# Performance work log

Hardware: AMD Instinct MI355X
Metric: run time of the kernel (lower is better)

Reference implementation:

```python
import jax, jax.numpy as jnp
import numpy as np

D_MODEL = 768
N_HEAD = 12

def setup_inputs() -> dict:
    key = jax.random.key(0)
    ks = jax.random.split(key, 5)
    B, T, C = 2, 2048, D_MODEL
    s = 1.0 / np.sqrt(C)
    x = jax.random.normal(ks[0], (B, T, C), dtype=jnp.float32)
    W_attn = jax.random.normal(ks[1], (C, 3 * C), dtype=jnp.float32) * s
    b_attn = jnp.zeros((3 * C,), dtype=jnp.float32)
    W_proj = jax.random.normal(ks[2], (C, C), dtype=jnp.float32) * s
    b_proj = jnp.zeros((C,), dtype=jnp.float32)
    return {"x": x, "W_attn": W_attn, "b_attn": b_attn, "W_proj": W_proj, "b_proj": b_proj}

def reference(x, W_attn, b_attn, W_proj, b_proj):
    B, T, C = x.shape
    H, Dh = N_HEAD, C // N_HEAD
    qkv = x @ W_attn + b_attn  # [B,T,3C]
    q, k, v = jnp.split(qkv, 3, axis=-1)
    q = q.reshape(B, T, H, Dh).transpose(0, 2, 1, 3)  # [B,H,T,Dh]
    k = k.reshape(B, T, H, Dh).transpose(0, 2, 1, 3)
    v = v.reshape(B, T, H, Dh).transpose(0, 2, 1, 3)
    att = jnp.einsum('bhqd,bhkd->bhqk', q, k) * (1.0 / np.sqrt(Dh))
    mask = jnp.tril(jnp.ones((T, T), dtype=bool))  # causal
    att = jnp.where(mask, att, -jnp.inf)
    att = jax.nn.softmax(att, axis=-1)
    y = jnp.einsum('bhqk,bhkd->bhqd', att, v)
    y = y.transpose(0, 2, 1, 3).reshape(B, T, C)
    return y @ W_proj + b_proj
```

## Files before the change

### kernel.cpp

```cpp
#include <hip/hip_runtime.h>
#include <hip/hip_bf16.h>
#include <math.h>

#define BB 2
#define TT 2048
#define CC 768
#define HH 12
#define DD 64
#define KD 768
#define NCH 80

#define QSCALE 0.18033688011112044f
#define THR2 11.5f

typedef __attribute__((ext_vector_type(8))) short bf16x8;
typedef __attribute__((ext_vector_type(4))) float f32x4;
typedef __attribute__((ext_vector_type(4))) float f32x4v;
typedef __attribute__((ext_vector_type(4))) ushort u16x4;

static __device__ __forceinline__ ushort f2bf(float f) {
  union { float f; unsigned u; } v; v.f = f;
  unsigned r = v.u + 0x7FFF + ((v.u >> 16) & 1);
  return (ushort)(r >> 16);
}
static __device__ __forceinline__ float bf2f(ushort u) {
  union { unsigned u; float f; } v; v.u = ((unsigned)u) << 16;
  return v.f;
}

#define NB_CVT 3072
#define NB_TA  1728
#define NB_TP  576

__global__ __launch_bounds__(256) void prep_fused(
    const float* __restrict__ x, ushort* __restrict__ xb,
    const float* __restrict__ Wa, ushort* __restrict__ Wat,
    const float* __restrict__ Wp, ushort* __restrict__ Wpt) {
  const int bid = blockIdx.x;
  const int tid = threadIdx.x;
  if (bid < NB_CVT) {
    const int i = bid * 256 + tid;
    f32x4v v = ((const f32x4v*)x)[i];
    u16x4 o;
    o.x = f2bf(v.x); o.y = f2bf(v.y); o.z = f2bf(v.z); o.w = f2bf(v.w);
    ((u16x4*)xb)[i] = o;
    return;
  }
  __shared__ float t[32][33];
  const float* W; ushort* Wt; int N, idx;
  if (bid < NB_CVT + NB_TA) { W = Wa; Wt = Wat; N = 3 * CC; idx = bid - NB_CVT; }
  else                      { W = Wp; Wt = Wpt; N = CC;     idx = bid - NB_CVT - NB_TA; }
  const int ntx = N / 32;
  const int n0 = (idx % ntx) * 32, k0 = (idx / ntx) * 32;
  const int tx = tid & 31, ty = tid >> 5;
#pragma unroll
  for (int j = 0; j < 32; j += 8)
    t[ty + j][tx] = W[(size_t)(k0 + ty + j) * N + n0 + tx];
  __syncthreads();
#pragma unroll
  for (int j = 0; j < 32; j += 8)
    Wt[(size_t)(n0 + ty + j) * KD + k0 + tx] = f2bf(t[tx][ty + j]);
}

__global__ __launch_bounds__(256) void gemm_mfma(
    const ushort* __restrict__ A, const ushort* __restrict__ Bt,
    const float* __restrict__ bias, int N, int mode,
    ushort* __restrict__ Qo, ushort* __restrict__ Ko, ushort* __restrict__ Vo,
    float* __restrict__ Of) {
  __shared__ ushort As[128 * 32];
  __shared__ ushort Bs[128 * 32];
  const int tid = threadIdx.x;
  const int w = tid >> 6, lane = tid & 63;
  const int wr = w >> 1, wc = w & 1;
  const int grp = lane >> 4, colk = lane & 15;
  const int bm = blockIdx.y * 128, bn = blockIdx.x * 128;

  f32x4 acc[4][4] = {};

  auto* AsL = (__attribute__((address_space(3))) char*)As;
  auto* BsL = (__attribute__((address_space(3))) char*)Bs;

  for (int k0 = 0; k0 < KD; k0 += 32) {
#pragma unroll
    for (int i = 0; i < 2; ++i) {
      const int idx = tid + i * 256;
      const int row = idx >> 2, g = idx & 3;
      const int eoff = (g * 8) ^ ((row & 3) << 3);
      const ushort* sa = A + (size_t)(bm + row) * KD + k0 + eoff;
      const ushort* sb = Bt + (size_t)(bn + row) * KD + k0 + eoff;
      __builtin_amdgcn_global_load_lds(
          (const __attribute__((address_space(1))) void*)sa,
          (__attribute__((address_space(3))) void*)(AsL + w * 1024 + i * 4096), 16, 0, 0);
      __builtin_amdgcn_global_load_lds(
          (const __attribute__((address_space(1))) void*)sb,
          (__attribute__((address_space(3))) void*)(BsL + w * 1024 + i * 4096), 16, 0, 0);
    }
    __syncthreads();

    bf16x8 af[4], bf[4];
    const int sw = (colk & 3) << 3;
#pragma unroll
    for (int m = 0; m < 4; ++m)
      af[m] = *(const bf16x8*)&As[(wr * 64 + m * 16 + colk) * 32 + ((grp * 8) ^ sw)];
#pragma unroll
    for (int n = 0; n < 4; ++n)
      bf[n] = *(const bf16x8*)&Bs[(wc * 64 + n * 16 + colk) * 32 + ((grp * 8) ^ sw)];
#pragma unroll
    for (int m = 0; m < 4; ++m)
#pragma unroll
      for (int n = 0; n < 4; ++n)
        acc[m][n] = __builtin_amdgcn_mfma_f32_16x16x32_bf16(af[m], bf[n], acc[m][n], 0, 0, 0);
    __syncthreads();
  }

#pragma unroll
  for (int m = 0; m < 4; ++m) {
    const int gro = bm + wr * 64 + m * 16 + grp * 4;
#pragma unroll
    for (int n = 0; n < 4; ++n) {
      const int col = bn + wc * 64 + n * 16 + colk;
      const float bv = bias[col];
#pragma unroll
      for (int j = 0; j < 4; ++j) {
        const int row = gro + j;
        float v = acc[m][n][j] + bv;
        if (mode == 0) {
          const int which = col / CC;
          const int c = col - which * CC;
          const int hh = c >> 6, d = c & 63;
          const int b = row >> 11, t = row & 2047;
          if (which == 0) v *= QSCALE;
          const ushort bvv = f2bf(v);
          if (which == 0)
            Qo[((size_t)((b * HH + hh) * TT + t)) * DD + d] = bvv;
          else if (which == 1)
            Ko[((size_t)((b * HH + hh) * TT + t)) * DD + d] = bvv;
          else
            Vo[((size_t)((b * HH + hh) * DD + d)) * TT + t] = bvv;
        } else {
          Of[(size_t)row * N + col] = v;
        }
      }
    }
  }
}

__global__ __launch_bounds__(256) void attn_mfma(
    const ushort* __restrict__ Q, const ushort* __restrict__ K,
    const ushort* __restrict__ Vt, ushort* __restrict__ Po,
    float* __restrict__ Pml) {
  const int c = NCH - 1 - (int)blockIdx.x;
  int qq, ci;
  if (c < 8)       { qq = c;                              ci = 0; }
  else if (c < 24) { int o_ = c - 8;  qq = 8  + (o_ >> 1); ci = o_ & 1; }
  else if (c < 48) { int o_ = c - 24; qq = 16 + o_ / 3;    ci = o_ % 3; }
  else             { int o_ = c - 48; qq = 24 + (o_ >> 2); ci = o_ & 3; }
  const int h = blockIdx.y, b = blockIdx.z;
  const int bh = b * HH + h;
  const size_t hb = (size_t)bh * TT * DD;
  const int kbase = ci * 512;
  const int nt = min(8, qq + 1 - ci * 8);

  __shared__ ushort Ks[64][72];
  __shared__ ushort Vs[64][72];
  __shared__ ushort Ps[4][16][72];
  __shared__ float scw[4][16];

  const int tid = threadIdx.x;
  const int w = tid >> 6, lane = tid & 63;
  const int grp = lane >> 4, colk = lane & 15;
  const int q0w = qq * 64 + w * 16;
  const int qme = q0w + colk;

  const ushort* Kg = K + hb;
  const ushort* Vg = Vt + hb;

  bf16x8 qf[2];
  {
    const ushort* qp = Q + hb + (size_t)(q0w + colk) * DD + 8 * grp;
    qf[0] = *(const bf16x8*)(qp);
    qf[1] = *(const bf16x8*)(qp + 32);
  }

  f32x4 o[4] = {};
  float m = -1e30f, l = 0.f;

  const int srow = tid >> 2;
  const int scol = (tid & 3) * 16;

  {
    bf16x8 k0a = *(const bf16x8*)&Kg[(size_t)(kbase + srow) * DD + scol];
    bf16x8 k0b = *(const bf16x8*)&Kg[(size_t)(kbase + srow) * DD + scol + 8];
    bf16x8 v0a = *(const bf16x8*)&Vg[(size_t)srow * TT + kbase + scol];
    bf16x8 v0b = *(const bf16x8*)&Vg[(size_t)srow * TT + kbase + scol + 8];
    *(bf16x8*)&Ks[srow][scol] = k0a;
    *(bf16x8*)&Ks[srow][scol + 8] = k0b;
    *(bf16x8*)&Vs[srow][scol] = v0a;
    *(bf16x8*)&Vs[srow][scol + 8] = v0b;
  }
  __syncthreads();

  for (int it = 0; it < nt; ++it) {
    const int k0 = kbase + it * 64;
    const bool pfn = (it + 1 < nt);
    bf16x8 nk0, nk1, nv0, nv1;
    if (pfn) {
      nk0 = *(const bf16x8*)&Kg[(size_t)(k0 + 64 + srow) * DD + scol];
      nk1 = *(const bf16x8*)&Kg[(size_t)(k0 + 64 + srow) * DD + scol + 8];
      nv0 = *(const bf16x8*)&Vg[(size_t)srow * TT + k0 + 64 + scol];
      nv1 = *(const bf16x8*)&Vg[(size_t)srow * TT + k0 + 64 + scol + 8];
    }

    f32x4 s2[4] = {};
    __builtin_amdgcn_s_setprio(1);
#pragma unroll
    for (int kb = 0; kb < 4; ++kb) {
      bf16x8 kf0 = *(const bf16x8*)&Ks[16 * kb + colk][8 * grp];
      bf16x8 kf1 = *(const bf16x8*)&Ks[16 * kb + colk][32 + 8 * grp];
      s2[kb] = __builtin_amdgcn_mfma_f32_16x16x32_bf16(kf0, qf[0], s2[kb], 0, 0, 0);
      s2[kb] = __builtin_amdgcn_mfma_f32_16x16x32_bf16(kf1, qf[1], s2[kb], 0, 0, 0);
    }
    __builtin_amdgcn_s_setprio(0);

    if (k0 + 63 > q0w) {
#pragma unroll
      for (int kb = 0; kb < 4; ++kb)
#pragma unroll
        for (int r = 0; r < 4; ++r)
          if (k0 + 16 * kb + 4 * grp + r > qme) s2[kb][r] = -1e30f;
    }
    float pm = -1e30f;
#pragma unroll
    for (int kb = 0; kb < 4; ++kb)
      pm = fmaxf(pm, fmaxf(fmaxf(s2[kb][0], s2[kb][1]), fmaxf(s2[kb][2], s2[kb][3])));
    pm = fmaxf(pm, __shfl_xor(pm, 16));
    pm = fmaxf(pm, __shfl_xor(pm, 32));

    if (__any(pm > m + THR2)) {
      const float mn = fmaxf(m, pm);
      const float sc = exp2f(m - mn);
      m = mn;
      l *= sc;
      if (grp == 0) scw[w][colk] = sc;
      const f32x4 s4 = *(const f32x4*)&scw[w][4 * grp];
#pragma unroll
      for (int n = 0; n < 4; ++n)
#pragma unroll
        for (int r = 0; r < 4; ++r) o[n][r] *= s4[r];
    }

    float ps = 0.f;
#pragma unroll
    for (int kb = 0; kb < 4; ++kb) {
      const float p0 = exp2f(s2[kb][0] - m);
      const float p1 = exp2f(s2[kb][1] - m);
      const float p2 = exp2f(s2[kb][2] - m);
      const float p3 = exp2f(s2[kb][3] - m);
      ps += (p0 + p1) + (p2 + p3);
      union { __hip_bfloat162 h2[2]; uint2 u2; } pk;
      pk.h2[0] = __float22bfloat162_rn(make_float2(p0, p1));
      pk.h2[1] = __float22bfloat162_rn(make_float2(p2, p3));
      *(uint2*)&Ps[w][colk][16 * kb + 4 * grp] = pk.u2;
    }
    ps += __shfl_xor(ps, 16);
    ps += __shfl_xor(ps, 32);
    l += ps;

    bf16x8 pf0 = *(const bf16x8*)&Ps[w][colk][8 * grp];
    bf16x8 pf1 = *(const bf16x8*)&Ps[w][colk][32 + 8 * grp];
    __builtin_amdgcn_s_setprio(1);
#pragma unroll
    for (int n = 0; n < 4; ++n) {
      bf16x8 vf0 = *(const bf16x8*)&Vs[16 * n + colk][8 * grp];
      bf16x8 vf1 = *(const bf16x8*)&Vs[16 * n + colk][32 + 8 * grp];
      o[n] = __builtin_amdgcn_mfma_f32_16x16x32_bf16(pf0, vf0, o[n], 0, 0, 0);
      o[n] = __builtin_amdgcn_mfma_f32_16x16x32_bf16(pf1, vf1, o[n], 0, 0, 0);
    }
    __builtin_amdgcn_s_setprio(0);

    if (pfn) {
      __syncthreads();
      *(bf16x8*)&Ks[srow][scol] = nk0;
      *(bf16x8*)&Ks[srow][scol + 8] = nk1;
      *(bf16x8*)&Vs[srow][scol] = nv0;
      *(bf16x8*)&Vs[srow][scol + 8] = nv1;
      __syncthreads();
    }
  }

  const size_t pbase = ((size_t)bh * NCH + c) * 64;
#pragma unroll
  for (int r = 0; r < 4; ++r) {
    const int row = w * 16 + grp * 4 + r;
#pragma unroll
    for (int n = 0; n < 4; ++n)
      Po[(pbase + row) * 64 + 16 * n + colk] = f2bf(o[n][r]);
  }
  if (grp == 0) {
    const int row = w * 16 + colk;
    Pml[(pbase + row) * 2] = m;
    Pml[(pbase + row) * 2 + 1] = l;
  }
}

__global__ __launch_bounds__(256) void attn_merge(
    const ushort* __restrict__ Po, const float* __restrict__ Pml,
    ushort* __restrict__ Yb) {
  const int qq = blockIdx.x, h = blockIdx.y, b = blockIdx.z;
  const int bh = b * HH + h;
  const int g = qq >> 3;
  const int nch = g + 1;
  const int gb = (g == 0) ? 0 : (g == 1) ? 8 : (g == 2) ? 24 : 48;
  const int cb = gb + nch * (qq - 8 * g);

  const int tid = threadIdx.x;
  const int row = tid >> 2;
  const int d0 = (tid & 3) * 16;

  float mi[4], li[4];
  float M = -1e30f;
#pragma unroll
  for (int i = 0; i < 4; ++i) {
    if (i < nch) {
      const size_t pb = ((size_t)bh * NCH + cb + i) * 64 + row;
      mi[i] = Pml[pb * 2];
      li[i] = Pml[pb * 2 + 1];
      M = fmaxf(M, mi[i]);
    }
  }
  float acc[16] = {};
  float lt = 0.f;
#pragma unroll
  for (int i = 0; i < 4; ++i) {
    if (i < nch) {
      const float wgt = exp2f(mi[i] - M);
      lt += li[i] * wgt;
      const ushort* pp = Po + (((size_t)bh * NCH + cb + i) * 64 + row) * 64 + d0;
      bf16x8 a = *(const bf16x8*)pp;
      bf16x8 bv = *(const bf16x8*)(pp + 8);
#pragma unroll
      for (int j = 0; j < 8; ++j) {
        acc[j] += wgt * bf2f((ushort)a[j]);
        acc[8 + j] += wgt * bf2f((ushort)bv[j]);
      }
    }
  }
  const float inv = 1.0f / lt;
  const int t = qq * 64 + row;
  ushort* yp = Yb + ((size_t)(b * TT) + t) * CC + h * DD + d0;
  bf16x8 o0, o1;
#pragma unroll
  for (int j = 0; j < 8; ++j) {
    o0[j] = (short)f2bf(acc[j] * inv);
    o1[j] = (short)f2bf(acc[8 + j] * inv);
  }
  *(bf16x8*)yp = o0;
  *(bf16x8*)(yp + 8) = o1;
}

extern "C" void kernel_launch(void* const* d_in, const int* in_sizes, int n_in,
                              void* d_out, int out_size, void* d_ws, size_t ws_size,
                              hipStream_t stream) {
  const float* x      = (const float*)d_in[0];
  const float* W_attn = (const float*)d_in[1];
  const float* b_attn = (const float*)d_in[2];
  const float* W_proj = (const float*)d_in[3];
  const float* b_proj = (const float*)d_in[4];
  float* out = (float*)d_out;

  const size_t per = (size_t)BB * TT * CC;
  ushort* Q   = (ushort*)d_ws;
  ushort* K   = Q + per;
  ushort* VtT = K + per;
  ushort* Yb  = VtT + per;
  ushort* Wpt = Yb + per;
  ushort* xb  = Wpt + (size_t)CC * CC;
  ushort* Wat = xb + per;
  ushort* Po  = xb;
  float*  Pml = (float*)(Po + (size_t)BB * HH * NCH * 64 * 64);

  prep_fused<<<dim3(NB_CVT + NB_TA + NB_TP), 256, 0, stream>>>(
      x, xb, W_attn, Wat, W_proj, Wpt);

  gemm_mfma<<<dim3(3 * CC / 128, BB * TT / 128), 256, 0, stream>>>(
      xb, Wat, b_attn, 3 * CC, 0, Q, K, VtT, nullptr);
  attn_mfma<<<dim3(NCH, HH, BB), 256, 0, stream>>>(Q, K, VtT, Po, Pml);
  attn_merge<<<dim3(TT / 64, HH, BB), 256, 0, stream>>>(Po, Pml, Yb);
  gemm_mfma<<<dim3(CC / 128, BB * TT / 128), 256, 0, stream>>>(
      Yb, Wpt, b_proj, CC, 1, nullptr, nullptr, nullptr, out);
}
```

Measured before the change: 119.4 us.

## Enlarge attention query tile to 128 rows with 512-thread blocks

Each attention block now handles 128 query rows with eight waves instead of 64 rows with four, halving the number of KV chunks and blocks. Each K/V tile staged in shared memory is reused by twice as many queries, and each thread loads half as much per tile. Waves whose query rows lie entirely before a KV tile skip its compute, which keeps the larger causal diagonal cheap. The trade-off is fewer blocks in the grid (960 rather than 1920) and more waves idling at barriers in diagonal tiles, and the merge kernel's indexing is updated to match.

```diff
diff --git a/kernel.cpp b/kernel.cpp
--- a/kernel.cpp
+++ b/kernel.cpp
@@ -8,7 +8,7 @@
 #define HH 12
 #define DD 64
 #define KD 768
-#define NCH 80
+#define NCH 40
 
 #define QSCALE 0.18033688011112044f
 #define THR2 11.5f
@@ -145,31 +145,31 @@
   }
 }
 
-__global__ __launch_bounds__(256) void attn_mfma(
+__global__ __launch_bounds__(512, 8) void attn_mfma(
     const ushort* __restrict__ Q, const ushort* __restrict__ K,
     const ushort* __restrict__ Vt, ushort* __restrict__ Po,
     float* __restrict__ Pml) {
   const int c = NCH - 1 - (int)blockIdx.x;
   int qq, ci;
-  if (c < 8)       { qq = c;                              ci = 0; }
-  else if (c < 24) { int o_ = c - 8;  qq = 8  + (o_ >> 1); ci = o_ & 1; }
-  else if (c < 48) { int o_ = c - 24; qq = 16 + o_ / 3;    ci = o_ % 3; }
-  else             { int o_ = c - 48; qq = 24 + (o_ >> 2); ci = o_ & 3; }
+  if (c < 4)       { qq = c;                               ci = 0; }
+  else if (c < 12) { int o_ = c - 4;  qq = 4  + (o_ >> 1); ci = o_ & 1; }
+  else if (c < 24) { int o_ = c - 12; qq = 8  + o_ / 3;    ci = o_ % 3; }
+  else             { int o_ = c - 24; qq = 12 + (o_ >> 2); ci = o_ & 3; }
   const int h = blockIdx.y, b = blockIdx.z;
   const int bh = b * HH + h;
   const size_t hb = (size_t)bh * TT * DD;
   const int kbase = ci * 512;
-  const int nt = min(8, qq + 1 - ci * 8);
+  const int nt = min(8, 2 * (qq + 1) - ci * 8);
 
   __shared__ ushort Ks[64][72];
   __shared__ ushort Vs[64][72];
-  __shared__ ushort Ps[4][16][72];
-  __shared__ float scw[4][16];
+  __shared__ ushort Ps[8][16][72];
+  __shared__ float scw[8][16];
 
   const int tid = threadIdx.x;
   const int w = tid >> 6, lane = tid & 63;
   const int grp = lane >> 4, colk = lane & 15;
-  const int q0w = qq * 64 + w * 16;
+  const int q0w = qq * 128 + w * 16;
   const int qme = q0w + colk;
 
   const ushort* Kg = K + hb;
@@ -185,110 +185,104 @@
   f32x4 o[4] = {};
   float m = -1e30f, l = 0.f;
 
-  const int srow = tid >> 2;
-  const int scol = (tid & 3) * 16;
+  const int srow = tid >> 3;
+  const int scol = (tid & 7) * 8;
 
   {
     bf16x8 k0a = *(const bf16x8*)&Kg[(size_t)(kbase + srow) * DD + scol];
-    bf16x8 k0b = *(const bf16x8*)&Kg[(size_t)(kbase + srow) * DD + scol + 8];
     bf16x8 v0a = *(const bf16x8*)&Vg[(size_t)srow * TT + kbase + scol];
-    bf16x8 v0b = *(const bf16x8*)&Vg[(size_t)srow * TT + kbase + scol + 8];
     *(bf16x8*)&Ks[srow][scol] = k0a;
-    *(bf16x8*)&Ks[srow][scol + 8] = k0b;
     *(bf16x8*)&Vs[srow][scol] = v0a;
-    *(bf16x8*)&Vs[srow][scol + 8] = v0b;
   }
   __syncthreads();
 
   for (int it = 0; it < nt; ++it) {
     const int k0 = kbase + it * 64;
     const bool pfn = (it + 1 < nt);
-    bf16x8 nk0, nk1, nv0, nv1;
+    bf16x8 nk0, nv0;
     if (pfn) {
       nk0 = *(const bf16x8*)&Kg[(size_t)(k0 + 64 + srow) * DD + scol];
-      nk1 = *(const bf16x8*)&Kg[(size_t)(k0 + 64 + srow) * DD + scol + 8];
       nv0 = *(const bf16x8*)&Vg[(size_t)srow * TT + k0 + 64 + scol];
-      nv1 = *(const bf16x8*)&Vg[(size_t)srow * TT + k0 + 64 + scol + 8];
-    }
-
-    f32x4 s2[4] = {};
-    __builtin_amdgcn_s_setprio(1);
-#pragma unroll
-    for (int kb = 0; kb < 4; ++kb) {
-      bf16x8 kf0 = *(const bf16x8*)&Ks[16 * kb + colk][8 * grp];
-      bf16x8 kf1 = *(const bf16x8*)&Ks[16 * kb + colk][32 + 8 * grp];
-      s2[kb] = __builtin_amdgcn_mfma_f32_16x16x32_bf16(kf0, qf[0], s2[kb], 0, 0, 0);
-      s2[kb] = __builtin_amdgcn_mfma_f32_16x16x32_bf16(kf1, qf[1], s2[kb], 0, 0, 0);
-    }
-    __builtin_amdgcn_s_setprio(0);
-
-    if (k0 + 63 > q0w) {
+    }
+
+    if (k0 <= q0w) {
+      f32x4 s2[4] = {};
+      __builtin_amdgcn_s_setprio(1);
+#pragma unroll
+      for (int kb = 0; kb < 4; ++kb) {
+        bf16x8 kf0 = *(const bf16x8*)&Ks[16 * kb + colk][8 * grp];
+        bf16x8 kf1 = *(const bf16x8*)&Ks[16 * kb + colk][32 + 8 * grp];
+        s2[kb] = __builtin_amdgcn_mfma_f32_16x16x32_bf16(kf0, qf[0], s2[kb], 0, 0, 0);
+        s2[kb] = __builtin_amdgcn_mfma_f32_16x16x32_bf16(kf1, qf[1], s2[kb], 0, 0, 0);
+      }
+      __builtin_amdgcn_s_setprio(0);
+
+      if (k0 + 63 > q0w) {
+#pragma unroll
+        for (int kb = 0; kb < 4; ++kb)
+#pragma unroll
+          for (int r = 0; r < 4; ++r)
+            if (k0 + 16 * kb + 4 * grp + r > qme) s2[kb][r] = -1e30f;
+      }
+      float pm = -1e30f;
 #pragma unroll
       for (int kb = 0; kb < 4; ++kb)
-#pragma unroll
-        for (int r = 0; r < 4; ++r)
-          if (k0 + 16 * kb + 4 * grp + r > qme) s2[kb][r] = -1e30f;
-    }
-    float pm = -1e30f;
-#pragma unroll
-    for (int kb = 0; kb < 4; ++kb)
-      pm = fmaxf(pm, fmaxf(fmaxf(s2[kb][0], s2[kb][1]), fmaxf(s2[kb][2], s2[kb][3])));
-    pm = fmaxf(pm, __shfl_xor(pm, 16));
-    pm = fmaxf(pm, __shfl_xor(pm, 32));
-
-    if (__any(pm > m + THR2)) {
-      const float mn = fmaxf(m, pm);
-      const float sc = exp2f(m - mn);
-      m = mn;
-      l *= sc;
-      if (grp == 0) scw[w][colk] = sc;
-      const f32x4 s4 = *(const f32x4*)&scw[w][4 * grp];
-#pragma unroll
-      for (int n = 0; n < 4; ++n)
-#pragma unroll
-        for (int r = 0; r < 4; ++r) o[n][r] *= s4[r];
-    }
-
-    float ps = 0.f;
-#pragma unroll
-    for (int kb = 0; kb < 4; ++kb) {
-      const float p0 = exp2f(s2[kb][0] - m);
-      const float p1 = exp2f(s2[kb][1] - m);
-      const float p2 = exp2f(s2[kb][2] - m);
-      const float p3 = exp2f(s2[kb][3] - m);
-      ps += (p0 + p1) + (p2 + p3);
-      union { __hip_bfloat162 h2[2]; uint2 u2; } pk;
-      pk.h2[0] = __float22bfloat162_rn(make_float2(p0, p1));
-      pk.h2[1] = __float22bfloat162_rn(make_float2(p2, p3));
-      *(uint2*)&Ps[w][colk][16 * kb + 4 * grp] = pk.u2;
-    }
-    ps += __shfl_xor(ps, 16);
-    ps += __shfl_xor(ps, 32);
-    l += ps;
-
-    bf16x8 pf0 = *(const bf16x8*)&Ps[w][colk][8 * grp];
-    bf16x8 pf1 = *(const bf16x8*)&Ps[w][colk][32 + 8 * grp];
-    __builtin_amdgcn_s_setprio(1);
-#pragma unroll
-    for (int n = 0; n < 4; ++n) {
-      bf16x8 vf0 = *(const bf16x8*)&Vs[16 * n + colk][8 * grp];
-      bf16x8 vf1 = *(const bf16x8*)&Vs[16 * n + colk][32 + 8 * grp];
-      o[n] = __builtin_amdgcn_mfma_f32_16x16x32_bf16(pf0, vf0, o[n], 0, 0, 0);
-      o[n] = __builtin_amdgcn_mfma_f32_16x16x32_bf16(pf1, vf1, o[n], 0, 0, 0);
-    }
-    __builtin_amdgcn_s_setprio(0);
+        pm = fmaxf(pm, fmaxf(fmaxf(s2[kb][0], s2[kb][1]), fmaxf(s2[kb][2], s2[kb][3])));
+      pm = fmaxf(pm, __shfl_xor(pm, 16));
+      pm = fmaxf(pm, __shfl_xor(pm, 32));
+
+      if (__any(pm > m + THR2)) {
+        const float mn = fmaxf(m, pm);
+        const float sc = exp2f(m - mn);
+        m = mn;
+        l *= sc;
+        if (grp == 0) scw[w][colk] = sc;
+        const f32x4 s4 = *(const f32x4*)&scw[w][4 * grp];
+#pragma unroll
+        for (int n = 0; n < 4; ++n)
+#pragma unroll
+          for (int r = 0; r < 4; ++r) o[n][r] *= s4[r];
+      }
+
+      float ps = 0.f;
+#pragma unroll
+      for (int kb = 0; kb < 4; ++kb) {
+        const float p0 = exp2f(s2[kb][0] - m);
+        const float p1 = exp2f(s2[kb][1] - m);
+        const float p2 = exp2f(s2[kb][2] - m);
+        const float p3 = exp2f(s2[kb][3] - m);
+        ps += (p0 + p1) + (p2 + p3);
+        union { __hip_bfloat162 h2[2]; uint2 u2; } pk;
+        pk.h2[0] = __float22bfloat162_rn(make_float2(p0, p1));
+        pk.h2[1] = __float22bfloat162_rn(make_float2(p2, p3));
+        *(uint2*)&Ps[w][colk][16 * kb + 4 * grp] = pk.u2;
+      }
+      ps += __shfl_xor(ps, 16);
+      ps += __shfl_xor(ps, 32);
+      l += ps;
+
+      bf16x8 pf0 = *(const bf16x8*)&Ps[w][colk][8 * grp];
+      bf16x8 pf1 = *(const bf16x8*)&Ps[w][colk][32 + 8 * grp];
+      __builtin_amdgcn_s_setprio(1);
+#pragma unroll
+      for (int n = 0; n < 4; ++n) {
+        bf16x8 vf0 = *(const bf16x8*)&Vs[16 * n + colk][8 * grp];
+        bf16x8 vf1 = *(const bf16x8*)&Vs[16 * n + colk][32 + 8 * grp];
+        o[n] = __builtin_amdgcn_mfma_f32_16x16x32_bf16(pf0, vf0, o[n], 0, 0, 0);
+        o[n] = __builtin_amdgcn_mfma_f32_16x16x32_bf16(pf1, vf1, o[n], 0, 0, 0);
+      }
+      __builtin_amdgcn_s_setprio(0);
+    }
 
     if (pfn) {
       __syncthreads();
       *(bf16x8*)&Ks[srow][scol] = nk0;
-      *(bf16x8*)&Ks[srow][scol + 8] = nk1;
       *(bf16x8*)&Vs[srow][scol] = nv0;
-      *(bf16x8*)&Vs[srow][scol + 8] = nv1;
       __syncthreads();
     }
   }
 
-  const size_t pbase = ((size_t)bh * NCH + c) * 64;
+  const size_t pbase = ((size_t)bh * NCH + c) * 128;
 #pragma unroll
   for (int r = 0; r < 4; ++r) {
     const int row = w * 16 + grp * 4 + r;
@@ -308,10 +302,12 @@
     ushort* __restrict__ Yb) {
   const int qq = blockIdx.x, h = blockIdx.y, b = blockIdx.z;
   const int bh = b * HH + h;
-  const int g = qq >> 3;
-  const int nch = g + 1;
-  const int gb = (g == 0) ? 0 : (g == 1) ? 8 : (g == 2) ? 24 : 48;
-  const int cb = gb + nch * (qq - 8 * g);
+  const int qh = qq >> 1;
+  const int gg = qh >> 2;
+  const int nch = gg + 1;
+  const int gb = (gg == 0) ? 0 : (gg == 1) ? 4 : (gg == 2) ? 12 : 24;
+  const int cb = gb + nch * (qh - 4 * gg);
+  const int rowo = (qq & 1) * 64;
 
   const int tid = threadIdx.x;
   const int row = tid >> 2;
@@ -322,7 +318,7 @@
 #pragma unroll
   for (int i = 0; i < 4; ++i) {
     if (i < nch) {
-      const size_t pb = ((size_t)bh * NCH + cb + i) * 64 + row;
+      const size_t pb = ((size_t)bh * NCH + cb + i) * 128 + rowo + row;
       mi[i] = Pml[pb * 2];
       li[i] = Pml[pb * 2 + 1];
       M = fmaxf(M, mi[i]);
@@ -335,7 +331,7 @@
     if (i < nch) {
       const float wgt = exp2f(mi[i] - M);
       lt += li[i] * wgt;
-      const ushort* pp = Po + (((size_t)bh * NCH + cb + i) * 64 + row) * 64 + d0;
+      const ushort* pp = Po + (((size_t)bh * NCH + cb + i) * 128 + rowo + row) * 64 + d0;
       bf16x8 a = *(const bf16x8*)pp;
       bf16x8 bv = *(const bf16x8*)(pp + 8);
 #pragma unroll
@@ -377,14 +373,14 @@
   ushort* xb  = Wpt + (size_t)CC * CC;
   ushort* Wat = xb + per;
   ushort* Po  = xb;
-  float*  Pml = (float*)(Po + (size_t)BB * HH * NCH * 64 * 64);
+  float*  Pml = (float*)(Po + (size_t)BB * HH * NCH * 128 * 64);
 
   prep_fused<<<dim3(NB_CVT + NB_TA + NB_TP), 256, 0, stream>>>(
       x, xb, W_attn, Wat, W_proj, Wpt);
 
   gemm_mfma<<<dim3(3 * CC / 128, BB * TT / 128), 256, 0, stream>>>(
       xb, Wat, b_attn, 3 * CC, 0, Q, K, VtT, nullptr);
-  attn_mfma<<<dim3(NCH, HH, BB), 256, 0, stream>>>(Q, K, VtT, Po, Pml);
+  attn_mfma<<<dim3(NCH, HH, BB), 512, 0, stream>>>(Q, K, VtT, Po, Pml);
   attn_merge<<<dim3(TT / 64, HH, BB), 256, 0, stream>>>(Po, Pml, Yb);
   gemm_mfma<<<dim3(CC / 128, BB * TT / 128), 256, 0, stream>>>(
       Yb, Wpt, b_proj, CC, 1, nullptr, nullptr, nullptr, out);
```

New measurement: 134.4 us. 1.13x slower.
